# Performance work log

Hardware: AMD Instinct MI355X
Metric: run time of the kernel (lower is better)

## Reference

```python
import jax, jax.numpy as jnp
import numpy as np

HIDDEN = 512
HEADS = 8
HEAD_DIM = HIDDEN // HEADS
TB_HID = 32  # temporal-bias MLP hidden width


def setup_inputs() -> dict:
    key = jax.random.key(0)
    ks = jax.random.split(key, 16)
    B, S, D = 4, 1024, HIDDEN
    s = 1.0 / np.sqrt(D)
    inp = {
        "query": jax.random.normal(ks[0], (B, S, D), jnp.float32),
        "key_": jax.random.normal(ks[1], (B, S, D), jnp.float32),
        "value": jax.random.normal(ks[2], (B, S, D), jnp.float32),
        "time_delta": jax.random.uniform(ks[3], (B, S, S), jnp.float32),
        "Wq": jax.random.normal(ks[4], (D, D), jnp.float32) * s,
        "bq": jnp.zeros((D,), jnp.float32),
        "Wk": jax.random.normal(ks[5], (D, D), jnp.float32) * s,
        "bk": jnp.zeros((D,), jnp.float32),
        "Wv": jax.random.normal(ks[6], (D, D), jnp.float32) * s,
        "bv": jnp.zeros((D,), jnp.float32),
        "Wo": jax.random.normal(ks[7], (D, D), jnp.float32) * s,
        "bo": jnp.zeros((D,), jnp.float32),
        "Wt1": jax.random.normal(ks[8], (1, TB_HID), jnp.float32),
        "bt1": jnp.zeros((TB_HID,), jnp.float32),
        "Wt2": jax.random.normal(ks[9], (TB_HID, HEADS), jnp.float32) * (1.0 / np.sqrt(TB_HID)),
        "bt2": jnp.zeros((HEADS,), jnp.float32),
    }
    return inp


def reference(query, key_, value, time_delta,
              Wq, bq, Wk, bk, Wv, bv, Wo, bo, Wt1, bt1, Wt2, bt2):
    B, S, D = query.shape
    H, Hd = HEADS, HEAD_DIM
    scale = jnp.sqrt(jnp.float32(Hd))

    # projections -> [B, H, S, Hd]
    q = (query @ Wq + bq).reshape(B, S, H, Hd).transpose(0, 2, 1, 3)
    k = (key_ @ Wk + bk).reshape(B, S, H, Hd).transpose(0, 2, 1, 3)
    v = (value @ Wv + bv).reshape(B, S, H, Hd).transpose(0, 2, 1, 3)

    # content scores [B, H, S, S]
    scores = jnp.einsum('bhid,bhjd->bhij', q, k) / scale

    # temporal bias: 2-layer MLP on scalar time_delta -> per-head bias
    h = jax.nn.relu(time_delta[..., None] * Wt1[0] + bt1)   # [B, S, S, 32]
    bias = h @ Wt2 + bt2                                    # [B, S, S, H]
    scores = scores + bias.transpose(0, 3, 1, 2)

    attn = jax.nn.softmax(scores, axis=-1)  # dropout = identity (eval)
    out = jnp.einsum('bhij,bhjd->bhid', attn, v)
    out = out.transpose(0, 2, 1, 3).reshape(B, S, D)
    return out @ Wo + bo
```

## Files before the change

### kernel.cpp

```cpp
#include <hip/hip_runtime.h>

typedef _Float16 f16;
typedef _Float16 f16x4 __attribute__((ext_vector_type(4)));
typedef _Float16 f16x8 __attribute__((ext_vector_type(8)));
typedef float f32x4 __attribute__((ext_vector_type(4)));

#define L2E 1.44269504088896340736f

constexpr int D  = 512;
constexpr int S  = 1024;
constexpr int B  = 4;
constexpr int BS = B * S;

constexpr size_t OFF_WT   = 0;
constexpr size_t OFF_Q16  = OFF_WT  + 4ull * D * D * 2;
constexpr size_t OFF_K16  = OFF_Q16 + (size_t)BS * D * 2;
constexpr size_t OFF_VT   = OFF_K16 + (size_t)BS * D * 2;
constexpr size_t OFF_AT   = OFF_VT  + (size_t)BS * D * 2;
constexpr size_t OFF_TAB  = OFF_AT  + (size_t)BS * D * 2;
constexpr size_t OFF_COEF = OFF_TAB + 8ull * 1032 * 4;
constexpr size_t OFF_TDH  = OFF_COEF + 256;

__global__ __launch_bounds__(256) void prep(
    const float* __restrict__ Wq, const float* __restrict__ Wk,
    const float* __restrict__ Wv, const float* __restrict__ Wo,
    f16* __restrict__ WT,
    const float* __restrict__ td, f16* __restrict__ tdh,
    const float* __restrict__ Wt1, const float* __restrict__ bt1,
    const float* __restrict__ Wt2, const float* __restrict__ bt2,
    float* __restrict__ tab, float* __restrict__ coef)
{
    __shared__ float tile[64][65];
    __shared__ float w1s[32], b1s[32], w2s[256], b2s[8];

    const int bx = blockIdx.x;
    const int t = threadIdx.x;

    if (bx < 256) {
        const int z = bx >> 6, xy = bx & 63;
        const float* __restrict__ W = (z == 0) ? Wq : (z == 1) ? Wk : (z == 2) ? Wv : Wo;
        f16* __restrict__ out = WT + (size_t)z * D * D;
        const int k0 = (xy >> 3) * 64, n0 = (xy & 7) * 64;
        for (int i = t; i < 4096; i += 256) {
            int r = i >> 6, c = i & 63;
            tile[r][c] = W[(size_t)(k0 + r) * D + n0 + c];
        }
        __syncthreads();
        for (int i = t; i < 4096; i += 256) {
            int nn = i >> 6, kk = i & 63;
            out[(size_t)(n0 + nn) * D + k0 + kk] = (f16)tile[kk][nn];
        }
    } else if (bx < 2304) {
        const int chunk = (bx - 256) * 256 + t;
        const int row = chunk >> 7;
        const int c7 = chunk & 127;
        const int tl = c7 >> 2, gg = c7 & 3;
        const float* __restrict__ src = td + (size_t)row * S + tl * 32;
        float4 a = *reinterpret_cast<const float4*>(src + gg * 4);
        float4 c = *reinterpret_cast<const float4*>(src + 16 + gg * 4);
        f16x8 hv;
        hv[0] = (f16)a.x; hv[1] = (f16)a.y; hv[2] = (f16)a.z; hv[3] = (f16)a.w;
        hv[4] = (f16)c.x; hv[5] = (f16)c.y; hv[6] = (f16)c.z; hv[7] = (f16)c.w;
        *reinterpret_cast<f16x8*>(tdh + (size_t)chunk * 8) = hv;
    } else {
        if (t < 32) { w1s[t] = Wt1[t]; b1s[t] = bt1[t]; }
        w2s[t] = Wt2[t];
        if (t < 8) b2s[t] = bt2[t];
        __syncthreads();

        const int hh = t >> 5, j = t & 31;

        float f0 = b2s[hh], f1 = b2s[hh];
#pragma unroll 4
        for (int jj = 0; jj < 32; ++jj) {
            float w2 = w2s[jj * 8 + hh];
            f0 += fmaxf(b1s[jj], 0.f) * w2;
            f1 += fmaxf(w1s[jj] + b1s[jj], 0.f) * w2;
        }

        float devj = 0.f;
        {
            float w1 = w1s[j], b1 = b1s[j];
            float u = (w1 != 0.f) ? (-b1 / w1) : -1.f;
            if (u > 0.f && u < 1.f) {
                float fu = b2s[hh];
#pragma unroll 4
                for (int jj = 0; jj < 32; ++jj)
                    fu += fmaxf(fmaf(u, w1s[jj], b1s[jj]), 0.f) * w2s[jj * 8 + hh];
                devj = fabsf(fu - fmaf(u, f1 - f0, f0)) * L2E;
            }
        }
#pragma unroll
        for (int m = 1; m < 32; m <<= 1)
            devj = fmaxf(devj, __shfl_xor(devj, m));

        if (j == 0) {
            coef[hh]     = (f1 - f0) * L2E;
            coef[8 + hh] = f0 * L2E;
            ((int*)coef)[16 + hh] = (devj < 1e-4f) ? 1 : 0;
        }

        for (int idx = t; idx <= 1024; idx += 256) {
            float tdv = (float)idx * (1.0f / 1024.0f);
            float acc[8];
#pragma unroll
            for (int h2 = 0; h2 < 8; ++h2) acc[h2] = b2s[h2];
#pragma unroll 4
            for (int jj = 0; jj < 32; ++jj) {
                float hvv = fmaxf(fmaf(tdv, w1s[jj], b1s[jj]), 0.f);
#pragma unroll
                for (int h2 = 0; h2 < 8; ++h2) acc[h2] += hvv * w2s[jj * 8 + h2];
            }
#pragma unroll
            for (int h2 = 0; h2 < 8; ++h2)
                tab[h2 * 1032 + idx] = acc[h2] * L2E;
        }
    }
}

__global__ __launch_bounds__(256) void proj_gemm(
    const float* __restrict__ Aq, const float* __restrict__ Ak, const float* __restrict__ Av,
    const f16* __restrict__ WT,
    const float* __restrict__ bq, const float* __restrict__ bk, const float* __restrict__ bv,
    f16* __restrict__ q16, f16* __restrict__ k16, f16* __restrict__ vT, float qscale)
{
    __shared__ f16 As[2][128][40];
    __shared__ f16 Bs[2][64][40];

    const int z = blockIdx.z;
    const float* __restrict__ A    = (z == 0) ? Aq : (z == 1) ? Ak : Av;
    const float* __restrict__ bias = (z == 0) ? bq : (z == 1) ? bk : bv;
    const f16* __restrict__ W      = WT + (size_t)z * D * D;
    const float scale = (z == 0) ? qscale : 1.0f;

    const int t = threadIdx.x;
    const int l = t & 63, w = t >> 6;
    const int i16 = l & 15, g = l >> 4;
    const int wm = w >> 1, wn = w & 1;
    const int m0 = blockIdx.x * 128, n0 = blockIdx.y * 64;

    f32x4 acc[4][2] = {};

    float4 ar[4];
    f16x8  br;
    const int arow = t >> 3, ac4 = t & 7;
    const int brow = t >> 2, bc8 = t & 3;

    auto load_stage = [&](int kt) {
        const int k0 = kt * 32;
#pragma unroll
        for (int r = 0; r < 4; ++r)
            ar[r] = *reinterpret_cast<const float4*>(A + (size_t)(m0 + arow + 32 * r) * D + k0 + ac4 * 4);
        br = *reinterpret_cast<const f16x8*>(W + (size_t)(n0 + brow) * D + k0 + bc8 * 8);
    };
    auto write_stage = [&](int buf) {
#pragma unroll
        for (int r = 0; r < 4; ++r) {
            f16x4 hv;
            hv[0] = (f16)ar[r].x; hv[1] = (f16)ar[r].y; hv[2] = (f16)ar[r].z; hv[3] = (f16)ar[r].w;
            *reinterpret_cast<f16x4*>(&As[buf][arow + 32 * r][ac4 * 4]) = hv;
        }
        *reinterpret_cast<f16x8*>(&Bs[buf][brow][bc8 * 8]) = br;
    };

    load_stage(0);
    write_stage(0);
    __syncthreads();

    for (int kt = 0; kt < 16; ++kt) {
        const int cur = kt & 1;
        if (kt < 15) load_stage(kt + 1);

        f16x8 af[4], bf[2];
#pragma unroll
        for (int i = 0; i < 4; ++i)
            af[i] = *reinterpret_cast<const f16x8*>(&As[cur][wm * 64 + i * 16 + i16][g * 8]);
#pragma unroll
        for (int j = 0; j < 2; ++j)
            bf[j] = *reinterpret_cast<const f16x8*>(&Bs[cur][wn * 32 + j * 16 + i16][g * 8]);
#pragma unroll
        for (int i = 0; i < 4; ++i)
#pragma unroll
            for (int j = 0; j < 2; ++j)
                acc[i][j] = __builtin_amdgcn_mfma_f32_16x16x32_f16(af[i], bf[j], acc[i][j], 0, 0, 0);

        if (kt < 15) write_stage(cur ^ 1);
        __syncthreads();
    }

    float bvv[2];
#pragma unroll
    for (int j = 0; j < 2; ++j) bvv[j] = bias[n0 + wn * 32 + j * 16 + i16];

    if (z < 2) {
        f16* __restrict__ out = (z == 0) ? q16 : k16;
#pragma unroll
        for (int i = 0; i < 4; ++i) {
#pragma unroll
            for (int j = 0; j < 2; ++j) {
                const int nn = n0 + wn * 32 + j * 16 + i16;
#pragma unroll
                for (int e = 0; e < 4; ++e) {
                    const int mr = m0 + wm * 64 + i * 16 + g * 4 + e;
                    out[(size_t)mr * D + nn] = (f16)((acc[i][j][e] + bvv[j]) * scale);
                }
            }
        }
    } else {
#pragma unroll
        for (int i = 0; i < 4; ++i) {
            const int mr = m0 + wm * 64 + i * 16 + g * 4;
            const int bb = mr >> 10, jj = mr & 1023;
#pragma unroll
            for (int j = 0; j < 2; ++j) {
                const int nn = n0 + wn * 32 + j * 16 + i16;
                f16x4 hv;
#pragma unroll
                for (int e = 0; e < 4; ++e) hv[e] = (f16)(acc[i][j][e] + bvv[j]);
                *reinterpret_cast<f16x4*>(vT + ((size_t)(bb * D + nn)) * S + jj) = hv;
            }
        }
    }
}

__global__ __launch_bounds__(256, 4) void attn_kernel(
    const f16* __restrict__ q16, const f16* __restrict__ k16, const f16* __restrict__ vT,
    const f16* __restrict__ tdh, const float* __restrict__ tabg, const float* __restrict__ coef,
    f16* __restrict__ out16)
{
    __shared__ __align__(16) f16 Ks[2][2][2048];
    __shared__ __align__(16) f16 Vs[2][2][2048];
    __shared__ __align__(16) f16 Ps[4][512];
    __shared__ float mlb[2][2][16];

    const int bid = blockIdx.x;
    const int b  = bid & 3;
    const int h  = (bid >> 2) & 7;
    const int qt = bid >> 5;

    const int t = threadIdx.x;
    const int w = t >> 6, l = t & 63;
    const int i16 = l & 15, g = l >> 4;
    const int half = w >> 1, pr = w & 1;
    const int qrow = qt * 32 + pr * 16 + i16;

    const float cH = coef[h], dH = coef[8 + h];
    const int lin = ((const int*)coef)[16 + h];
    const float* __restrict__ th = tabg + h * 1032;

    f16x8 qf[2];
#pragma unroll
    for (int kf = 0; kf < 2; ++kf)
        qf[kf] = *reinterpret_cast<const f16x8*>(
            q16 + (size_t)(b * S + qrow) * D + h * 64 + kf * 32 + g * 8);

    float mr = -1e30f, lr = 0.f;
    f32x4 o[4] = {};

    const int krow = t >> 3, kc8 = t & 7;
    const int vdv  = t >> 2, vj8 = t & 3;
    const int kofs = krow * 64 + ((kc8 ^ (krow & 7)) << 3);
    const int vofs = vdv * 32 + ((vj8 ^ (vdv & 3)) << 3);
    f16x8 sk0, sk1, sv0, sv1;

    auto stage_load = [&](int jt) {
        const f16* kp = k16 + (size_t)(b * S + jt * 32 + krow) * D + h * 64 + kc8 * 8;
        sk0 = *reinterpret_cast<const f16x8*>(kp);
        sk1 = *reinterpret_cast<const f16x8*>(kp + (size_t)512 * D);
        const f16* vp = vT + (size_t)(b * D + h * 64 + vdv) * S + jt * 32 + vj8 * 8;
        sv0 = *reinterpret_cast<const f16x8*>(vp);
        sv1 = *reinterpret_cast<const f16x8*>(vp + 512);
    };
    auto stage_write = [&](int buf) {
        *reinterpret_cast<f16x8*>(&Ks[buf][0][kofs]) = sk0;
        *reinterpret_cast<f16x8*>(&Ks[buf][1][kofs]) = sk1;
        *reinterpret_cast<f16x8*>(&Vs[buf][0][vofs]) = sv0;
        *reinterpret_cast<f16x8*>(&Vs[buf][1][vofs]) = sv1;
    };

    int kro0[2], kro1[2], vro[4];
#pragma unroll
    for (int fj = 0; fj < 2; ++fj) {
        const int rj = fj * 16 + i16;
        kro0[fj] = rj * 64 + ((g ^ (i16 & 7)) << 3);
        kro1[fj] = rj * 64 + (((g + 4) ^ (i16 & 7)) << 3);
    }
#pragma unroll
    for (int fv = 0; fv < 4; ++fv)
        vro[fv] = (fv * 16 + i16) * 32 + ((g ^ (i16 & 3)) << 3);

    const int q2  = (i16 >> 1) & 3;
    const int pw0 = i16 * 32 + ((((g >> 1)    ) ^ q2) << 3) + ((g & 1) << 2);
    const int pw1 = i16 * 32 + ((((g >> 1) + 2) ^ q2) << 3) + ((g & 1) << 2);
    const int prd = i16 * 32 + ((g ^ q2) << 3);

    const f16* __restrict__ tdp = tdh + (size_t)(b * S + qrow) * S + half * 512 + g * 8;
    f16x8 tcur, tnext;

    stage_load(0);
    tcur = *reinterpret_cast<const f16x8*>(tdp);
    stage_write(0);
    __syncthreads();

    for (int jt = 0; jt < 16; ++jt) {
        const int cur = jt & 1;
        if (jt < 15) {
            stage_load(jt + 1);
            tnext = *reinterpret_cast<const f16x8*>(tdp + (jt + 1) * 32);
        }

        f32x4 s[2];
#pragma unroll
        for (int fj = 0; fj < 2; ++fj) {
            f16x8 ka0 = *reinterpret_cast<const f16x8*>(&Ks[cur][half][kro0[fj]]);
            f16x8 ka1 = *reinterpret_cast<const f16x8*>(&Ks[cur][half][kro1[fj]]);
            f32x4 zz = {0.f, 0.f, 0.f, 0.f};
            zz = __builtin_amdgcn_mfma_f32_16x16x32_f16(ka0, qf[0], zz, 0, 0, 0);
            s[fj] = __builtin_amdgcn_mfma_f32_16x16x32_f16(ka1, qf[1], zz, 0, 0, 0);
        }

        float pvv[2][4];
        float tmax = -1e30f;
#pragma unroll
        for (int fj = 0; fj < 2; ++fj)
#pragma unroll
            for (int e = 0; e < 4; ++e) {
                float u = (float)tcur[fj * 4 + e];
                float vsc;
                if (lin) {
                    vsc = fmaf(u, cH, s[fj][e] + dH);
                } else {
                    float x = fminf(fmaxf(u, 0.f), 1.f) * 1024.f;
                    int ix = (int)x;
                    ix = (ix > 1023) ? 1023 : ix;
                    float fr = x - (float)ix;
                    float t0v = th[ix], t1v = th[ix + 1];
                    vsc = s[fj][e] + fmaf(fr, t1v - t0v, t0v);
                }
                pvv[fj][e] = vsc;
                tmax = fmaxf(tmax, vsc);
            }
        tmax = fmaxf(tmax, __shfl_xor(tmax, 16));
        tmax = fmaxf(tmax, __shfl_xor(tmax, 32));
        if (__any(tmax > mr)) {
            float mnew = fmaxf(mr, tmax);
            float alpha = exp2f(mr - mnew);
            mr = mnew;
            lr *= alpha;
#pragma unroll
            for (int fv = 0; fv < 4; ++fv) o[fv] *= alpha;
        }

        float rsum = 0.f;
        f16x4 pq[2];
#pragma unroll
        for (int fj = 0; fj < 2; ++fj)
#pragma unroll
            for (int e = 0; e < 4; ++e) {
                float p = exp2f(pvv[fj][e] - mr);
                rsum += p;
                pq[fj][e] = (f16)p;
            }
        rsum += __shfl_xor(rsum, 16);
        rsum += __shfl_xor(rsum, 32);
        lr += rsum;

        f16* ps = Ps[w];
        *reinterpret_cast<f16x4*>(ps + pw0) = pq[0];
        *reinterpret_cast<f16x4*>(ps + pw1) = pq[1];
        f16x8 pb = *reinterpret_cast<const f16x8*>(ps + prd);

#pragma unroll
        for (int fv = 0; fv < 4; ++fv) {
            f16x8 va = *reinterpret_cast<const f16x8*>(&Vs[cur][half][vro[fv]]);
            o[fv] = __builtin_amdgcn_mfma_f32_16x16x32_f16(va, pb, o[fv], 0, 0, 0);
        }

        if (jt < 15) stage_write(cur ^ 1);
        __syncthreads();
        tcur = tnext;
    }

    float* ob = (float*)&Ks[0][0][0];
    if (w >= 2) {
        float* obp = ob + pr * (16 * 68);
#pragma unroll
        for (int fv = 0; fv < 4; ++fv)
            *reinterpret_cast<f32x4*>(&obp[i16 * 68 + fv * 16 + g * 4]) = o[fv];
        if (g == 0) { mlb[pr][0][i16] = mr; mlb[pr][1][i16] = lr; }
    }
    __syncthreads();
    if (w < 2) {
        const float m1 = mlb[pr][0][i16], l1 = mlb[pr][1][i16];
        const float mm = fmaxf(mr, m1);
        const float a0 = exp2f(mr - mm), a1 = exp2f(m1 - mm);
        const float inv = 1.0f / (lr * a0 + l1 * a1);
        const float* obp = ob + pr * (16 * 68);
#pragma unroll
        for (int fv = 0; fv < 4; ++fv) {
            f32x4 o1 = *reinterpret_cast<const f32x4*>(&obp[i16 * 68 + fv * 16 + g * 4]);
            f16x4 hv;
#pragma unroll
            for (int e = 0; e < 4; ++e) hv[e] = (f16)((o[fv][e] * a0 + o1[e] * a1) * inv);
            *reinterpret_cast<f16x4*>(
                out16 + (size_t)(b * S + qrow) * D + h * 64 + fv * 16 + g * 4) = hv;
        }
    }
}

__global__ __launch_bounds__(256) void final_gemm(const f16* __restrict__ A, const f16* __restrict__ WoT,
                                                  const float* __restrict__ bo, float* __restrict__ out)
{
    __shared__ f16 As[2][64][40];
    __shared__ f16 Bs[2][64][40];

    const int t = threadIdx.x;
    const int l = t & 63, w = t >> 6;
    const int i16 = l & 15, g = l >> 4;
    const int wm = w >> 1, wn = w & 1;
    const int m0 = blockIdx.x * 64, n0 = blockIdx.y * 64;

    f32x4 acc[2][2] = {};
    f16x8 ar, br;
    const int srow = t >> 2, sc8 = t & 3;

    auto load_stage = [&](int kt) {
        const int k0 = kt * 32;
        ar = *reinterpret_cast<const f16x8*>(A + (size_t)(m0 + srow) * D + k0 + sc8 * 8);
        br = *reinterpret_cast<const f16x8*>(WoT + (size_t)(n0 + srow) * D + k0 + sc8 * 8);
    };
    auto write_stage = [&](int buf) {
        *reinterpret_cast<f16x8*>(&As[buf][srow][sc8 * 8]) = ar;
        *reinterpret_cast<f16x8*>(&Bs[buf][srow][sc8 * 8]) = br;
    };

    load_stage(0);
    write_stage(0);
    __syncthreads();

    for (int kt = 0; kt < 16; ++kt) {
        const int cur = kt & 1;
        if (kt < 15) load_stage(kt + 1);

        f16x8 af[2], bf[2];
#pragma unroll
        for (int i = 0; i < 2; ++i)
            af[i] = *reinterpret_cast<const f16x8*>(&As[cur][wm * 32 + i * 16 + i16][g * 8]);
#pragma unroll
        for (int j = 0; j < 2; ++j)
            bf[j] = *reinterpret_cast<const f16x8*>(&Bs[cur][wn * 32 + j * 16 + i16][g * 8]);
#pragma unroll
        for (int i = 0; i < 2; ++i)
#pragma unroll
            for (int j = 0; j < 2; ++j)
                acc[i][j] = __builtin_amdgcn_mfma_f32_16x16x32_f16(af[i], bf[j], acc[i][j], 0, 0, 0);

        if (kt < 15) write_stage(cur ^ 1);
        __syncthreads();
    }

    float bvv[2];
#pragma unroll
    for (int j = 0; j < 2; ++j) bvv[j] = bo[n0 + wn * 32 + j * 16 + i16];

#pragma unroll
    for (int i = 0; i < 2; ++i) {
#pragma unroll
        for (int j = 0; j < 2; ++j) {
            const int nn = n0 + wn * 32 + j * 16 + i16;
#pragma unroll
            for (int e = 0; e < 4; ++e) {
                const int mr = m0 + wm * 32 + i * 16 + g * 4 + e;
                out[(size_t)mr * D + nn] = acc[i][j][e] + bvv[j];
            }
        }
    }
}

extern "C" void kernel_launch(void* const* d_in, const int* in_sizes, int n_in,
                              void* d_out, int out_size, void* d_ws, size_t ws_size,
                              hipStream_t stream)
{
    (void)in_sizes; (void)n_in; (void)out_size; (void)ws_size;

    const float* query = (const float*)d_in[0];
    const float* key_  = (const float*)d_in[1];
    const float* value = (const float*)d_in[2];
    const float* td    = (const float*)d_in[3];
    const float* Wq  = (const float*)d_in[4];  const float* bq  = (const float*)d_in[5];
    const float* Wk  = (const float*)d_in[6];  const float* bk  = (const float*)d_in[7];
    const float* Wv  = (const float*)d_in[8];  const float* bv  = (const float*)d_in[9];
    const float* Wo  = (const float*)d_in[10]; const float* bo  = (const float*)d_in[11];
    const float* Wt1 = (const float*)d_in[12]; const float* bt1 = (const float*)d_in[13];
    const float* Wt2 = (const float*)d_in[14]; const float* bt2 = (const float*)d_in[15];
    float* out = (float*)d_out;

    char* ws = (char*)d_ws;
    f16*   WT   = (f16*)(ws + OFF_WT);
    f16*   q16  = (f16*)(ws + OFF_Q16);
    f16*   k16  = (f16*)(ws + OFF_K16);
    f16*   vT   = (f16*)(ws + OFF_VT);
    f16*   at16 = (f16*)(ws + OFF_AT);
    float* tab  = (float*)(ws + OFF_TAB);
    float* coef = (float*)(ws + OFF_COEF);
    f16*   tdh  = (f16*)(ws + OFF_TDH);

    prep<<<2305, 256, 0, stream>>>(Wq, Wk, Wv, Wo, WT, td, tdh,
                                   Wt1, bt1, Wt2, bt2, tab, coef);
    proj_gemm<<<dim3(32, 8, 3), 256, 0, stream>>>(query, key_, value, WT, bq, bk, bv,
                                                  q16, k16, vT, 0.125f * L2E);
    attn_kernel<<<1024, 256, 0, stream>>>(q16, k16, vT, tdh, tab, coef, at16);
    final_gemm<<<dim3(64, 8), 256, 0, stream>>>(at16, WT + 3ull * (size_t)D * D, bo, out);
}
```

Measured before the change: 74.49 us.

## Deepen attention K/V prefetch to two tiles ahead with unrolled ping-pong

```diff
diff --git a/kernel.cpp b/kernel.cpp
--- a/kernel.cpp
+++ b/kernel.cpp
@@ -261,21 +261,21 @@
     const int vdv  = t >> 2, vj8 = t & 3;
     const int kofs = krow * 64 + ((kc8 ^ (krow & 7)) << 3);
     const int vofs = vdv * 32 + ((vj8 ^ (vdv & 3)) << 3);
-    f16x8 sk0, sk1, sv0, sv1;
-
-    auto stage_load = [&](int jt) {
+
+    auto loadSet = [&](f16x8& k0r, f16x8& k1r, f16x8& v0r, f16x8& v1r, int jt) {
         const f16* kp = k16 + (size_t)(b * S + jt * 32 + krow) * D + h * 64 + kc8 * 8;
-        sk0 = *reinterpret_cast<const f16x8*>(kp);
-        sk1 = *reinterpret_cast<const f16x8*>(kp + (size_t)512 * D);
+        k0r = *reinterpret_cast<const f16x8*>(kp);
+        k1r = *reinterpret_cast<const f16x8*>(kp + (size_t)512 * D);
         const f16* vp = vT + (size_t)(b * D + h * 64 + vdv) * S + jt * 32 + vj8 * 8;
-        sv0 = *reinterpret_cast<const f16x8*>(vp);
-        sv1 = *reinterpret_cast<const f16x8*>(vp + 512);
-    };
-    auto stage_write = [&](int buf) {
-        *reinterpret_cast<f16x8*>(&Ks[buf][0][kofs]) = sk0;
-        *reinterpret_cast<f16x8*>(&Ks[buf][1][kofs]) = sk1;
-        *reinterpret_cast<f16x8*>(&Vs[buf][0][vofs]) = sv0;
-        *reinterpret_cast<f16x8*>(&Vs[buf][1][vofs]) = sv1;
+        v0r = *reinterpret_cast<const f16x8*>(vp);
+        v1r = *reinterpret_cast<const f16x8*>(vp + 512);
+    };
+    auto writeSet = [&](int buf, const f16x8& k0r, const f16x8& k1r,
+                        const f16x8& v0r, const f16x8& v1r) {
+        *reinterpret_cast<f16x8*>(&Ks[buf][0][kofs]) = k0r;
+        *reinterpret_cast<f16x8*>(&Ks[buf][1][kofs]) = k1r;
+        *reinterpret_cast<f16x8*>(&Vs[buf][0][vofs]) = v0r;
+        *reinterpret_cast<f16x8*>(&Vs[buf][1][vofs]) = v1r;
     };
 
     int kro0[2], kro1[2], vro[4];
@@ -295,20 +295,8 @@
     const int prd = i16 * 32 + ((g ^ q2) << 3);
 
     const f16* __restrict__ tdp = tdh + (size_t)(b * S + qrow) * S + half * 512 + g * 8;
-    f16x8 tcur, tnext;
-
-    stage_load(0);
-    tcur = *reinterpret_cast<const f16x8*>(tdp);
-    stage_write(0);
-    __syncthreads();
-
-    for (int jt = 0; jt < 16; ++jt) {
-        const int cur = jt & 1;
-        if (jt < 15) {
-            stage_load(jt + 1);
-            tnext = *reinterpret_cast<const f16x8*>(tdp + (jt + 1) * 32);
-        }
-
+
+    auto tile = [&](int cur, f16x8 tcur) {
         f32x4 s[2];
 #pragma unroll
         for (int fj = 0; fj < 2; ++fj) {
@@ -375,10 +363,39 @@
             f16x8 va = *reinterpret_cast<const f16x8*>(&Vs[cur][half][vro[fv]]);
             o[fv] = __builtin_amdgcn_mfma_f32_16x16x32_f16(va, pb, o[fv], 0, 0, 0);
         }
-
-        if (jt < 15) stage_write(cur ^ 1);
-        __syncthreads();
-        tcur = tnext;
+    };
+
+    f16x8 skE0, skE1, svE0, svE1, skO0, skO1, svO0, svO1;
+    f16x8 tE, tO;
+
+    loadSet(skE0, skE1, svE0, svE1, 0);
+    tE = *reinterpret_cast<const f16x8*>(tdp);
+    writeSet(0, skE0, skE1, svE0, svE1);
+    loadSet(skO0, skO1, svO0, svO1, 1);
+    tO = *reinterpret_cast<const f16x8*>(tdp + 32);
+    __syncthreads();
+
+    for (int p = 0; p < 8; ++p) {
+        {
+            f16x8 tcur = tE;
+            if (p < 7) {
+                loadSet(skE0, skE1, svE0, svE1, 2 * p + 2);
+                tE = *reinterpret_cast<const f16x8*>(tdp + (2 * p + 2) * 32);
+            }
+            tile(0, tcur);
+            writeSet(1, skO0, skO1, svO0, svO1);
+            __syncthreads();
+        }
+        {
+            f16x8 tcur = tO;
+            if (p < 7) {
+                loadSet(skO0, skO1, svO0, svO1, 2 * p + 3);
+                tO = *reinterpret_cast<const f16x8*>(tdp + (2 * p + 3) * 32);
+            }
+            tile(1, tcur);
+            if (p < 7) writeSet(0, skE0, skE1, svE0, svE1);
+            __syncthreads();
+        }
     }
 
     float* ob = (float*)&Ks[0][0][0];
```

New measurement: 74.75 us. About the same (+0.3%).

## Widen attention blocks to 64 query rows with 8 waves sharing K/V tiles

Applied to the files above, without the earlier changes.

```diff
diff --git a/kernel.cpp b/kernel.cpp
--- a/kernel.cpp
+++ b/kernel.cpp
@@ -223,15 +223,16 @@
     }
 }
 
-__global__ __launch_bounds__(256, 4) void attn_kernel(
+__global__ __launch_bounds__(512, 4) void attn_kernel(
     const f16* __restrict__ q16, const f16* __restrict__ k16, const f16* __restrict__ vT,
     const f16* __restrict__ tdh, const float* __restrict__ tabg, const float* __restrict__ coef,
     f16* __restrict__ out16)
 {
     __shared__ __align__(16) f16 Ks[2][2][2048];
     __shared__ __align__(16) f16 Vs[2][2][2048];
-    __shared__ __align__(16) f16 Ps[4][512];
-    __shared__ float mlb[2][2][16];
+    __shared__ __align__(16) f16 Ps[8][512];
+    __shared__ float obuf[4][16][68];
+    __shared__ float mlb[4][2][16];
 
     const int bid = blockIdx.x;
     const int b  = bid & 3;
@@ -241,8 +242,8 @@
     const int t = threadIdx.x;
     const int w = t >> 6, l = t & 63;
     const int i16 = l & 15, g = l >> 4;
-    const int half = w >> 1, pr = w & 1;
-    const int qrow = qt * 32 + pr * 16 + i16;
+    const int half = w >> 2, pr = w & 3;
+    const int qrow = qt * 64 + pr * 16 + i16;
 
     const float cH = coef[h], dH = coef[8 + h];
     const int lin = ((const int*)coef)[16 + h];
@@ -257,25 +258,22 @@
     float mr = -1e30f, lr = 0.f;
     f32x4 o[4] = {};
 
-    const int krow = t >> 3, kc8 = t & 7;
-    const int vdv  = t >> 2, vj8 = t & 3;
+    const int kh   = t >> 8;
+    const int krow = (t >> 3) & 31, kc8 = t & 7;
+    const int vdv  = (t >> 2) & 63, vj8 = t & 3;
     const int kofs = krow * 64 + ((kc8 ^ (krow & 7)) << 3);
     const int vofs = vdv * 32 + ((vj8 ^ (vdv & 3)) << 3);
-    f16x8 sk0, sk1, sv0, sv1;
+    f16x8 sk, sv;
 
     auto stage_load = [&](int jt) {
-        const f16* kp = k16 + (size_t)(b * S + jt * 32 + krow) * D + h * 64 + kc8 * 8;
-        sk0 = *reinterpret_cast<const f16x8*>(kp);
-        sk1 = *reinterpret_cast<const f16x8*>(kp + (size_t)512 * D);
-        const f16* vp = vT + (size_t)(b * D + h * 64 + vdv) * S + jt * 32 + vj8 * 8;
-        sv0 = *reinterpret_cast<const f16x8*>(vp);
-        sv1 = *reinterpret_cast<const f16x8*>(vp + 512);
+        sk = *reinterpret_cast<const f16x8*>(
+            k16 + (size_t)(b * S + kh * 512 + jt * 32 + krow) * D + h * 64 + kc8 * 8);
+        sv = *reinterpret_cast<const f16x8*>(
+            vT + (size_t)(b * D + h * 64 + vdv) * S + kh * 512 + jt * 32 + vj8 * 8);
     };
     auto stage_write = [&](int buf) {
-        *reinterpret_cast<f16x8*>(&Ks[buf][0][kofs]) = sk0;
-        *reinterpret_cast<f16x8*>(&Ks[buf][1][kofs]) = sk1;
-        *reinterpret_cast<f16x8*>(&Vs[buf][0][vofs]) = sv0;
-        *reinterpret_cast<f16x8*>(&Vs[buf][1][vofs]) = sv1;
+        *reinterpret_cast<f16x8*>(&Ks[buf][kh][kofs]) = sk;
+        *reinterpret_cast<f16x8*>(&Vs[buf][kh][vofs]) = sv;
     };
 
     int kro0[2], kro1[2], vro[4];
@@ -381,24 +379,21 @@
         tcur = tnext;
     }
 
-    float* ob = (float*)&Ks[0][0][0];
-    if (w >= 2) {
-        float* obp = ob + pr * (16 * 68);
+    if (half == 1) {
 #pragma unroll
         for (int fv = 0; fv < 4; ++fv)
-            *reinterpret_cast<f32x4*>(&obp[i16 * 68 + fv * 16 + g * 4]) = o[fv];
+            *reinterpret_cast<f32x4*>(&obuf[pr][i16][fv * 16 + g * 4]) = o[fv];
         if (g == 0) { mlb[pr][0][i16] = mr; mlb[pr][1][i16] = lr; }
     }
     __syncthreads();
-    if (w < 2) {
+    if (half == 0) {
         const float m1 = mlb[pr][0][i16], l1 = mlb[pr][1][i16];
         const float mm = fmaxf(mr, m1);
         const float a0 = exp2f(mr - mm), a1 = exp2f(m1 - mm);
         const float inv = 1.0f / (lr * a0 + l1 * a1);
-        const float* obp = ob + pr * (16 * 68);
 #pragma unroll
         for (int fv = 0; fv < 4; ++fv) {
-            f32x4 o1 = *reinterpret_cast<const f32x4*>(&obp[i16 * 68 + fv * 16 + g * 4]);
+            f32x4 o1 = *reinterpret_cast<const f32x4*>(&obuf[pr][i16][fv * 16 + g * 4]);
             f16x4 hv;
 #pragma unroll
             for (int e = 0; e < 4; ++e) hv[e] = (f16)((o[fv][e] * a0 + o1[e] * a1) * inv);
@@ -509,6 +504,6 @@
                                    Wt1, bt1, Wt2, bt2, tab, coef);
     proj_gemm<<<dim3(32, 8, 3), 256, 0, stream>>>(query, key_, value, WT, bq, bk, bv,
                                                   q16, k16, vT, 0.125f * L2E);
-    attn_kernel<<<1024, 256, 0, stream>>>(q16, k16, vT, tdh, tab, coef, at16);
+    attn_kernel<<<512, 512, 0, stream>>>(q16, k16, vT, tdh, tab, coef, at16);
     final_gemm<<<dim3(64, 8), 256, 0, stream>>>(at16, WT + 3ull * (size_t)D * D, bo, out);
 }
```

Result: faster. 71.76 us (-3.7%).
